# Kernel optimization log

Hardware: AMD Instinct MI355X
Metric: run time of the kernel (lower is better)

Reference implementation:

```python
import jax, jax.numpy as jnp
import numpy as np

N_NODES = 50000
N_EDGES = 800000
IN_FEATS = 128
HIDDEN = 128
NUM_CLASSES = 47


def setup_inputs() -> dict:
    key = jax.random.key(0)
    k1, k2, k3, k4 = jax.random.split(key, 4)
    features = jax.random.normal(k1, (N_NODES, IN_FEATS), dtype=jnp.float32)
    edge_index = jax.random.randint(k2, (2, N_EDGES), 0, N_NODES, dtype=jnp.int32)
    # Glorot-style init for weights, zeros for bias (DGL GraphConv defaults)
    W1 = jax.random.normal(k3, (IN_FEATS, HIDDEN), dtype=jnp.float32) * (1.0 / np.sqrt(IN_FEATS))
    b1 = jnp.zeros((HIDDEN,), dtype=jnp.float32)
    W2 = jax.random.normal(k4, (HIDDEN, NUM_CLASSES), dtype=jnp.float32) * (1.0 / np.sqrt(HIDDEN))
    b2 = jnp.zeros((NUM_CLASSES,), dtype=jnp.float32)
    return {"features": features, "edge_index": edge_index,
            "W1": W1, "b1": b1, "W2": W2, "b2": b2}


def _graph_conv(x, W, b, src, dst, norm_src, norm_dst, n_nodes):
    # DGL GraphConv, norm='both': D_dst^{-1/2} A D_src^{-1/2} (X W) + b
    h = (x * norm_src[:, None]) @ W            # transform before aggregation
    agg = jax.ops.segment_sum(h[src], dst, num_segments=n_nodes)
    return agg * norm_dst[:, None] + b


def reference(features, edge_index, W1, b1, W2, b2):
    src, dst = edge_index[0], edge_index[1]
    n = features.shape[0]
    ones = jnp.ones((src.shape[0],), dtype=features.dtype)
    deg_out = jax.ops.segment_sum(ones, src, num_segments=n)
    deg_in = jax.ops.segment_sum(ones, dst, num_segments=n)
    norm_src = jax.lax.rsqrt(jnp.clip(deg_out, 1.0))   # d_out^{-1/2}, clamp >= 1
    norm_dst = jax.lax.rsqrt(jnp.clip(deg_in, 1.0))    # d_in^{-1/2}, clamp >= 1

    h = _graph_conv(features, W1, b1, src, dst, norm_src, norm_dst, n)
    h = jax.nn.relu(h)
    out = _graph_conv(h, W2, b2, src, dst, norm_src, norm_dst, n)
    return out
```

## Files before the change

kernel.cpp:

```cpp
#include <hip/hip_runtime.h>
#include <hip/hip_fp16.h>

#define N_NODES 50000
#define N_EDGES 800000
#define IN_F 128
#define HID 128
#define NCLS 47
#define H2S 48
#define W2C 64
#define NCH 196
#define NB 128
#define CHUNK 6250
#define PDW 12500
#define G1ROWS 256
#define G2ROWS 128


typedef _Float16 f16x8 __attribute__((ext_vector_type(8)));
typedef float f32x4 __attribute__((ext_vector_type(4)));

struct __align__(8)  h2x2 { __half2 a, b; };
struct __align__(16) h2x4 { __half2 a, b, c, d; };

__global__ __launch_bounds__(256) void prep_kernel(const float* __restrict__ W1,
                                                   const float* __restrict__ W2,
                                                   __half* __restrict__ W1Th,
                                                   __half* __restrict__ W1Tl,
                                                   __half* __restrict__ W2Th,
                                                   __half* __restrict__ W2Tl) {
    const int b = blockIdx.x, t = threadIdx.x;
    if (b < 32) {
        const int i0 = b * 512;
        for (int i2 = i0 + t; i2 < i0 + 512; i2 += 256) {
            int cc = i2 >> 7, k = i2 & 127;
            float w = W1[k * HID + cc];
            __half hv = __float2half_rn(w);
            W1Th[i2] = hv;
            W1Tl[i2] = __float2half_rn(w - __half2float(hv));
        }
    } else {
        const int i0 = (b - 32) * 512;
        for (int i2 = i0 + t; i2 < i0 + 512; i2 += 256) {
            int cc = i2 >> 7, k = i2 & 127;
            float w = (cc < NCLS) ? W2[k * NCLS + cc] : 0.f;
            __half hv = __float2half_rn(w);
            W2Th[i2] = hv;
            W2Tl[i2] = __float2half_rn(w - __half2float(hv));
        }
    }
}

__global__ __launch_bounds__(512) void hist_gemm1_kernel(const int* __restrict__ ei,
        unsigned int* __restrict__ Pdst, unsigned int* __restrict__ Psrc,
        const float* __restrict__ X, const __half* __restrict__ W1Th,
        const __half* __restrict__ W1Tl, __half* __restrict__ H1h) {
    __shared__ unsigned int h[PDW];
    const int t = threadIdx.x;
    if (blockIdx.x < 2 * NB) {
        const bool is_src = blockIdx.x >= NB;
        const int chunk = blockIdx.x & (NB - 1);
        const int* ids = is_src ? ei : ei + N_EDGES;
        uint2* h2 = (uint2*)h;
        for (int j = t; j < PDW / 2; j += 512) h2[j] = make_uint2(0u, 0u);
        __syncthreads();
        const int e0 = chunk * CHUNK;
        const int2* e2p = (const int2*)(ids + e0);
        for (int k = t; k < CHUNK / 2; k += 512) {
            int2 v2 = e2p[k];
            atomicAdd(&h[v2.x >> 2], 1u << ((v2.x & 3) * 8));
            atomicAdd(&h[v2.y >> 2], 1u << ((v2.y & 3) * 8));
        }
        __syncthreads();
        unsigned int* P = (is_src ? Psrc : Pdst) + (size_t)chunk * PDW;
        uint2* P2 = (uint2*)P;
        for (int j = t; j < PDW / 2; j += 512) P2[j] = h2[j];
    } else {
        const int lane = t & 63;
        const int wv = t >> 6;
        const int r16 = lane & 15;
        const int kg = lane >> 4;
        const int row0 = (blockIdx.x - 2 * NB) * G1ROWS + wv * 32;
        f32x4 acc[2][8] = {};
#pragma unroll
        for (int s = 0; s < 4; ++s) {
            const int k0 = 32 * s + 8 * kg;
            f16x8 ah[2], al[2];
#pragma unroll
            for (int rt = 0; rt < 2; ++rt) {
                int row = row0 + rt * 16 + r16;
                int rc = row < N_NODES ? row : N_NODES - 1;
                const float4 x0 = *(const float4*)&X[(size_t)rc * IN_F + k0];
                const float4 x1 = *(const float4*)&X[(size_t)rc * IN_F + k0 + 4];
                const float xv[8] = {x0.x, x0.y, x0.z, x0.w,
                                     x1.x, x1.y, x1.z, x1.w};
#pragma unroll
                for (int j = 0; j < 8; ++j) {
                    _Float16 hv = (_Float16)xv[j];
                    ah[rt][j] = hv;
                    al[rt][j] = (_Float16)(xv[j] - (float)hv);
                }
            }
#pragma unroll
            for (int tt = 0; tt < 8; ++tt) {
                const f16x8 bh = *(const f16x8*)&W1Th[(16 * tt + r16) * IN_F + k0];
                const f16x8 bl = *(const f16x8*)&W1Tl[(16 * tt + r16) * IN_F + k0];
#pragma unroll
                for (int rt = 0; rt < 2; ++rt) {
                    acc[rt][tt] = __builtin_amdgcn_mfma_f32_16x16x32_f16(
                        ah[rt], bh, acc[rt][tt], 0, 0, 0);
                    acc[rt][tt] = __builtin_amdgcn_mfma_f32_16x16x32_f16(
                        al[rt], bh, acc[rt][tt], 0, 0, 0);
                    acc[rt][tt] = __builtin_amdgcn_mfma_f32_16x16x32_f16(
                        ah[rt], bl, acc[rt][tt], 0, 0, 0);
                }
            }
        }
#pragma unroll
        for (int rt = 0; rt < 2; ++rt)
#pragma unroll
            for (int j = 0; j < 4; ++j) {
                const int row = row0 + rt * 16 + 4 * kg + j;
                if (row < N_NODES) {
#pragma unroll
                    for (int tt = 0; tt < 8; ++tt)
                        H1h[(size_t)row * HID + 16 * tt + r16] =
                            __float2half_rn(acc[rt][tt][j]);
                }
            }
    }
}

__global__ __launch_bounds__(256) void reduce_kernel(unsigned int* __restrict__ Pdst,
                                                     const unsigned int* __restrict__ Psrc,
                                                     int* __restrict__ cnt_in,
                                                     float* __restrict__ norm_src,
                                                     float* __restrict__ norm_dst,
                                                     int* __restrict__ chunk_sums) {
    __shared__ int sm[256];
    const int t = threadIdx.x;
    const int j = blockIdx.x * 256 + t;
    int tot = 0;
    if (j < PDW) {
        unsigned int run = 0;
#pragma unroll 8
        for (int b = 0; b < NB; ++b) {
            unsigned int v = Pdst[(size_t)b * PDW + j];
            Pdst[(size_t)b * PDW + j] = run;
            run += v;
        }
        int n0 = run & 0xff, n1 = (run >> 8) & 0xff;
        int n2 = (run >> 16) & 0xff, n3 = (run >> 24) & 0xff;
        *(int4*)&cnt_in[4 * j] = make_int4(n0, n1, n2, n3);
        *(float4*)&norm_dst[4 * j] = make_float4(
            rsqrtf(fmaxf((float)n0, 1.0f)), rsqrtf(fmaxf((float)n1, 1.0f)),
            rsqrtf(fmaxf((float)n2, 1.0f)), rsqrtf(fmaxf((float)n3, 1.0f)));
        tot = n0 + n1 + n2 + n3;
        unsigned int rs = 0;
#pragma unroll 8
        for (int b = 0; b < NB; ++b) rs += Psrc[(size_t)b * PDW + j];
        int s0 = rs & 0xff, s1 = (rs >> 8) & 0xff;
        int s2 = (rs >> 16) & 0xff, s3 = (rs >> 24) & 0xff;
        *(float4*)&norm_src[4 * j] = make_float4(
            rsqrtf(fmaxf((float)s0, 1.0f)), rsqrtf(fmaxf((float)s1, 1.0f)),
            rsqrtf(fmaxf((float)s2, 1.0f)), rsqrtf(fmaxf((float)s3, 1.0f)));
    }
    sm[t] = tot;
    __syncthreads();
    const int g = t & 63;
    for (int off = 32; off > 0; off >>= 1) {
        if (g < off) sm[t] += sm[t + off];
        __syncthreads();
    }
    if (g == 0) chunk_sums[blockIdx.x * 4 + (t >> 6)] = sm[t];
}

__global__ __launch_bounds__(256) void scan3_kernel(const int* __restrict__ cnt_in,
                                                    const int* __restrict__ chunk_sums,
                                                    int* __restrict__ offsets) {
    __shared__ int sm[256];
    const int t = threadIdx.x;
    int v = (t < NCH) ? chunk_sums[t] : 0;
    sm[t] = v;
    __syncthreads();
    for (int off = 1; off < 256; off <<= 1) {
        int u = (t >= off) ? sm[t - off] : 0;
        __syncthreads();
        sm[t] += u;
        __syncthreads();
    }
    const int basev = (blockIdx.x == 0) ? 0 : sm[blockIdx.x - 1];
    __syncthreads();
    const int idx = blockIdx.x * 256 + t;
    int c = (idx < N_NODES) ? cnt_in[idx] : 0;
    sm[t] = c;
    __syncthreads();
    for (int off = 1; off < 256; off <<= 1) {
        int u = (t >= off) ? sm[t - off] : 0;
        __syncthreads();
        sm[t] += u;
        __syncthreads();
    }
    if (idx < N_NODES) offsets[idx] = basev + sm[t] - c;
    if (blockIdx.x == 0 && t == 0) offsets[N_NODES] = N_EDGES;
}

__global__ __launch_bounds__(512) void fill_kernel(const int* __restrict__ src,
        const int* __restrict__ dst, const int* __restrict__ offsets,
        const unsigned int* __restrict__ Pdst, int* __restrict__ csr_src) {
    __shared__ __align__(16) unsigned int cur[PDW];
    const int t = threadIdx.x;
    const int chunk = blockIdx.x;
    uint2* c2 = (uint2*)cur;
    for (int j = t; j < PDW / 2; j += 512) c2[j] = make_uint2(0u, 0u);
    __syncthreads();
    const unsigned int* base = Pdst + (size_t)chunk * PDW;
    const int e0 = chunk * CHUNK;
    const int2* d2p = (const int2*)(dst + e0);
    const int2* s2p = (const int2*)(src + e0);
    for (int k = t; k < CHUNK / 2; k += 512) {
        int2 d2 = d2p[k];
        int2 s2 = s2p[k];
        {
            const int d = d2.x;
            const int sh = (d & 3) * 8;
            const unsigned int bw = base[d >> 2];
            const int off = offsets[d];
            unsigned int old = atomicAdd(&cur[d >> 2], 1u << sh);
            csr_src[off + (int)((bw >> sh) & 0xffu) + (int)((old >> sh) & 0xffu)] = s2.x;
        }
        {
            const int d = d2.y;
            const int sh = (d & 3) * 8;
            const unsigned int bw = base[d >> 2];
            const int off = offsets[d];
            unsigned int old = atomicAdd(&cur[d >> 2], 1u << sh);
            csr_src[off + (int)((bw >> sh) & 0xffu) + (int)((old >> sh) & 0xffu)] = s2.y;
        }
    }
}

__global__ __launch_bounds__(256) void gather1_kernel(const __half* __restrict__ H1h,
        const int* __restrict__ offsets, const int* __restrict__ csr_src,
        const float* __restrict__ b1, const float* __restrict__ norm_src,
        const float* __restrict__ norm_dst, __half* __restrict__ Hrelu16) {
    const int lane = threadIdx.x & 63;
    const int q = lane >> 4;
    const int fl = lane & 15;
    const int row = blockIdx.x * 4 + (threadIdx.x >> 6);
    const int beg = offsets[row], end = offsets[row + 1];
    float a0 = 0.f, a1 = 0.f, a2 = 0.f, a3 = 0.f;
    float a4 = 0.f, a5 = 0.f, a6 = 0.f, a7 = 0.f;
    for (int base = beg; base < end; base += 64) {
        int idx = 0;
        float nsv = 0.f;
        if (base + lane < end) {
            idx = csr_src[base + lane];
            nsv = norm_src[idx];
        }
        const int cnt = min(end - base, 64);
        for (int j = 0; j < cnt; j += 16) {
            int e0 = j + q, e1 = j + 4 + q, e2 = j + 8 + q, e3 = j + 12 + q;
            int s0 = __shfl(idx, e0);  float n0 = __shfl(nsv, e0);
            int s1 = __shfl(idx, e1);  float n1 = __shfl(nsv, e1);
            int s2 = __shfl(idx, e2);  float n2 = __shfl(nsv, e2);
            int s3 = __shfl(idx, e3);  float n3 = __shfl(nsv, e3);
            h2x4 v0 = *(const h2x4*)&H1h[(size_t)s0 * HID + 8 * fl];
            h2x4 v1 = *(const h2x4*)&H1h[(size_t)s1 * HID + 8 * fl];
            h2x4 v2 = *(const h2x4*)&H1h[(size_t)s2 * HID + 8 * fl];
            h2x4 v3 = *(const h2x4*)&H1h[(size_t)s3 * HID + 8 * fl];
            float2 f;
            f = __half22float2(v0.a); a0 = fmaf(f.x, n0, a0); a1 = fmaf(f.y, n0, a1);
            f = __half22float2(v0.b); a2 = fmaf(f.x, n0, a2); a3 = fmaf(f.y, n0, a3);
            f = __half22float2(v0.c); a4 = fmaf(f.x, n0, a4); a5 = fmaf(f.y, n0, a5);
            f = __half22float2(v0.d); a6 = fmaf(f.x, n0, a6); a7 = fmaf(f.y, n0, a7);
            f = __half22float2(v1.a); a0 = fmaf(f.x, n1, a0); a1 = fmaf(f.y, n1, a1);
            f = __half22float2(v1.b); a2 = fmaf(f.x, n1, a2); a3 = fmaf(f.y, n1, a3);
            f = __half22float2(v1.c); a4 = fmaf(f.x, n1, a4); a5 = fmaf(f.y, n1, a5);
            f = __half22float2(v1.d); a6 = fmaf(f.x, n1, a6); a7 = fmaf(f.y, n1, a7);
            f = __half22float2(v2.a); a0 = fmaf(f.x, n2, a0); a1 = fmaf(f.y, n2, a1);
            f = __half22float2(v2.b); a2 = fmaf(f.x, n2, a2); a3 = fmaf(f.y, n2, a3);
            f = __half22float2(v2.c); a4 = fmaf(f.x, n2, a4); a5 = fmaf(f.y, n2, a5);
            f = __half22float2(v2.d); a6 = fmaf(f.x, n2, a6); a7 = fmaf(f.y, n2, a7);
            f = __half22float2(v3.a); a0 = fmaf(f.x, n3, a0); a1 = fmaf(f.y, n3, a1);
            f = __half22float2(v3.b); a2 = fmaf(f.x, n3, a2); a3 = fmaf(f.y, n3, a3);
            f = __half22float2(v3.c); a4 = fmaf(f.x, n3, a4); a5 = fmaf(f.y, n3, a5);
            f = __half22float2(v3.d); a6 = fmaf(f.x, n3, a6); a7 = fmaf(f.y, n3, a7);
        }
    }
    a0 += __shfl_xor(a0, 16); a1 += __shfl_xor(a1, 16);
    a2 += __shfl_xor(a2, 16); a3 += __shfl_xor(a3, 16);
    a4 += __shfl_xor(a4, 16); a5 += __shfl_xor(a5, 16);
    a6 += __shfl_xor(a6, 16); a7 += __shfl_xor(a7, 16);
    a0 += __shfl_xor(a0, 32); a1 += __shfl_xor(a1, 32);
    a2 += __shfl_xor(a2, 32); a3 += __shfl_xor(a3, 32);
    a4 += __shfl_xor(a4, 32); a5 += __shfl_xor(a5, 32);
    a6 += __shfl_xor(a6, 32); a7 += __shfl_xor(a7, 32);
    if (lane < 16) {
        float nd = norm_dst[row], ns = norm_src[row];
        float4 bA = *(const float4*)&b1[8 * fl];
        float4 bB = *(const float4*)&b1[8 * fl + 4];
        float o0 = fmaxf(fmaf(a0, nd, bA.x), 0.f) * ns;
        float o1 = fmaxf(fmaf(a1, nd, bA.y), 0.f) * ns;
        float o2 = fmaxf(fmaf(a2, nd, bA.z), 0.f) * ns;
        float o3 = fmaxf(fmaf(a3, nd, bA.w), 0.f) * ns;
        float o4 = fmaxf(fmaf(a4, nd, bB.x), 0.f) * ns;
        float o5 = fmaxf(fmaf(a5, nd, bB.y), 0.f) * ns;
        float o6 = fmaxf(fmaf(a6, nd, bB.z), 0.f) * ns;
        float o7 = fmaxf(fmaf(a7, nd, bB.w), 0.f) * ns;
        h2x4 p = {__floats2half2_rn(o0, o1), __floats2half2_rn(o2, o3),
                  __floats2half2_rn(o4, o5), __floats2half2_rn(o6, o7)};
        *(h2x4*)&Hrelu16[(size_t)row * HID + 8 * fl] = p;
    }
}

__global__ __launch_bounds__(256) void gemm2_kernel(const __half* __restrict__ Hrelu16,
                                                    const __half* __restrict__ W2Th,
                                                    const __half* __restrict__ W2Tl,
                                                    __half* __restrict__ H2h) {
    const int lane = threadIdx.x & 63;
    const int wv = threadIdx.x >> 6;
    const int r16 = lane & 15;
    const int kg = lane >> 4;
    const int row0 = blockIdx.x * G2ROWS + wv * 32;
    f32x4 acc[2][3] = {};
#pragma unroll
    for (int s = 0; s < 4; ++s) {
        const int k0 = 32 * s + 8 * kg;
        f16x8 a[2];
#pragma unroll
        for (int rt = 0; rt < 2; ++rt) {
            int row = row0 + rt * 16 + r16;
            int rc = row < N_NODES ? row : N_NODES - 1;
            a[rt] = *(const f16x8*)&Hrelu16[(size_t)rc * HID + k0];
        }
#pragma unroll
        for (int tt = 0; tt < 3; ++tt) {
            const f16x8 bh = *(const f16x8*)&W2Th[(16 * tt + r16) * HID + k0];
            const f16x8 bl = *(const f16x8*)&W2Tl[(16 * tt + r16) * HID + k0];
#pragma unroll
            for (int rt = 0; rt < 2; ++rt) {
                acc[rt][tt] = __builtin_amdgcn_mfma_f32_16x16x32_f16(
                    a[rt], bh, acc[rt][tt], 0, 0, 0);
                acc[rt][tt] = __builtin_amdgcn_mfma_f32_16x16x32_f16(
                    a[rt], bl, acc[rt][tt], 0, 0, 0);
            }
        }
    }
#pragma unroll
    for (int rt = 0; rt < 2; ++rt)
#pragma unroll
        for (int j = 0; j < 4; ++j) {
            const int row = row0 + rt * 16 + 4 * kg + j;
            if (row < N_NODES) {
#pragma unroll
                for (int tt = 0; tt < 3; ++tt)
                    H2h[(size_t)row * H2S + 16 * tt + r16] =
                        __float2half_rn(acc[rt][tt][j]);
            }
        }
}

__global__ __launch_bounds__(256) void gather2_kernel(const __half* __restrict__ H2h,
        const int* __restrict__ offsets, const int* __restrict__ csr_src,
        const float* __restrict__ b2, const float* __restrict__ norm_dst,
        float* __restrict__ out) {
    const int lane = threadIdx.x & 63;
    const int row = blockIdx.x * 4 + (threadIdx.x >> 6);
    const int beg = offsets[row], end = offsets[row + 1];
    const int cl = min(lane, H2S - 1);
    float acc = 0.f;
    for (int base = beg; base < end; base += 64) {
        int idx = 0;
        float wv = 0.f;
        if (base + lane < end) {
            idx = csr_src[base + lane];
            wv = 1.f;
        }
        const int cnt = min(end - base, 64);
        for (int j = 0; j < cnt; j += 4) {
            int s0 = __shfl(idx, j);     float w0 = __shfl(wv, j);
            int s1 = __shfl(idx, j + 1); float w1 = __shfl(wv, j + 1);
            int s2 = __shfl(idx, j + 2); float w2 = __shfl(wv, j + 2);
            int s3 = __shfl(idx, j + 3); float w3 = __shfl(wv, j + 3);
            float f0 = __half2float(H2h[(size_t)s0 * H2S + cl]);
            float f1 = __half2float(H2h[(size_t)s1 * H2S + cl]);
            float f2 = __half2float(H2h[(size_t)s2 * H2S + cl]);
            float f3 = __half2float(H2h[(size_t)s3 * H2S + cl]);
            acc = fmaf(f0, w0, acc);
            acc = fmaf(f1, w1, acc);
            acc = fmaf(f2, w2, acc);
            acc = fmaf(f3, w3, acc);
        }
    }
    if (lane < NCLS) out[(size_t)row * NCLS + lane] = acc * norm_dst[row] + b2[lane];
}

extern "C" void kernel_launch(void* const* d_in, const int* in_sizes, int n_in,
                              void* d_out, int out_size, void* d_ws, size_t ws_size,
                              hipStream_t stream) {
    const float* X  = (const float*)d_in[0];
    const int*   ei = (const int*)d_in[1];
    const float* W1 = (const float*)d_in[2];
    const float* b1 = (const float*)d_in[3];
    const float* W2 = (const float*)d_in[4];
    const float* b2 = (const float*)d_in[5];
    float* out = (float*)d_out;

    const int* src = ei;
    const int* dst = ei + N_EDGES;

    char* w = (char*)d_ws;
    auto alloc = [&](size_t bytes) {
        char* p = w;
        w += (bytes + 255) & ~(size_t)255;
        return p;
    };
    float*  norm_src   = (float*)alloc(N_NODES * 4);
    float*  norm_dst   = (float*)alloc(N_NODES * 4);
    int*    cnt_in     = (int*)alloc(N_NODES * 4);
    int*    offsets    = (int*)alloc((N_NODES + 1) * 4);
    int*    csr_src    = (int*)alloc((size_t)N_EDGES * 4);
    int*    chunk_sums = (int*)alloc(NCH * 4);
    __half* W1Th       = (__half*)alloc((size_t)IN_F * HID * 2);
    __half* W1Tl       = (__half*)alloc((size_t)IN_F * HID * 2);
    __half* W2Th       = (__half*)alloc((size_t)W2C * HID * 2);
    __half* W2Tl       = (__half*)alloc((size_t)W2C * HID * 2);
    __half* H1h        = (__half*)alloc((size_t)N_NODES * HID * 2);
    __half* Hrelu16    = (__half*)alloc((size_t)N_NODES * HID * 2);
    __half* H2h        = (__half*)alloc((size_t)N_NODES * H2S * 2);
    unsigned int* Pdst = (unsigned int*)alloc((size_t)NB * PDW * 4);
    unsigned int* Psrc = (unsigned int*)alloc((size_t)NB * PDW * 4);

    const int g1_blocks = (N_NODES + G1ROWS - 1) / G1ROWS;
    const int g2_blocks = (N_NODES + G2ROWS - 1) / G2ROWS;
    prep_kernel<<<48, 256, 0, stream>>>(W1, W2, W1Th, W1Tl, W2Th, W2Tl);
    hist_gemm1_kernel<<<2 * NB + g1_blocks, 512, 0, stream>>>(ei, Pdst, Psrc,
                                                              X, W1Th, W1Tl, H1h);
    reduce_kernel<<<(PDW + 255) / 256, 256, 0, stream>>>(Pdst, Psrc, cnt_in,
                                                         norm_src, norm_dst, chunk_sums);
    scan3_kernel<<<NCH, 256, 0, stream>>>(cnt_in, chunk_sums, offsets);
    fill_kernel<<<NB, 512, 0, stream>>>(src, dst, offsets, Pdst, csr_src);
    gather1_kernel<<<N_NODES / 4, 256, 0, stream>>>(H1h, offsets, csr_src, b1,
                                                    norm_src, norm_dst, Hrelu16);
    gemm2_kernel<<<g2_blocks, 256, 0, stream>>>(Hrelu16, W2Th, W2Tl, H2h);
    gather2_kernel<<<N_NODES / 4, 256, 0, stream>>>(H2h, offsets, csr_src, b2,
                                                    norm_dst, out);
}
```

Measured before the change: 207.2 us.

## Replace chunked shared-memory histograms with global atomic degree count and cursor fill

Drops the per-chunk packed 8-bit shared-memory histograms and their partial-sum reduction. Degrees are now counted with global atomics, and the CSR is filled through a per-node cursor taken from the prefix scan. The fill is fused with GEMM1, which now applies norm_src before storing, so gather1 no longer loads norm_src per edge. This removes large Pdst/Psrc traffic and a reduce pass, in exchange for heavy contention on global atomics and a non-deterministic neighbor order in the CSR.

```diff
diff --git a/kernel.cpp b/kernel.cpp
--- a/kernel.cpp
+++ b/kernel.cpp
@@ -9,12 +9,10 @@
 #define H2S 48
 #define W2C 64
 #define NCH 196
-#define NB 128
-#define CHUNK 6250
-#define PDW 12500
 #define G1ROWS 256
 #define G2ROWS 128
-
+#define DEGB 128
+#define FILLB 256
 
 typedef _Float16 f16x8 __attribute__((ext_vector_type(8)));
 typedef float f32x4 __attribute__((ext_vector_type(4)));
@@ -22,161 +20,72 @@
 struct __align__(8)  h2x2 { __half2 a, b; };
 struct __align__(16) h2x4 { __half2 a, b, c, d; };
 
-__global__ __launch_bounds__(256) void prep_kernel(const float* __restrict__ W1,
-                                                   const float* __restrict__ W2,
-                                                   __half* __restrict__ W1Th,
-                                                   __half* __restrict__ W1Tl,
-                                                   __half* __restrict__ W2Th,
-                                                   __half* __restrict__ W2Tl) {
-    const int b = blockIdx.x, t = threadIdx.x;
-    if (b < 32) {
-        const int i0 = b * 512;
-        for (int i2 = i0 + t; i2 < i0 + 512; i2 += 256) {
-            int cc = i2 >> 7, k = i2 & 127;
-            float w = W1[k * HID + cc];
-            __half hv = __float2half_rn(w);
-            W1Th[i2] = hv;
-            W1Tl[i2] = __float2half_rn(w - __half2float(hv));
+__global__ __launch_bounds__(512) void deg_prep_kernel(const int* __restrict__ ei,
+        int* __restrict__ deg_in, int* __restrict__ deg_out,
+        const float* __restrict__ W1, const float* __restrict__ W2,
+        __half* __restrict__ W1Th, __half* __restrict__ W1Tl,
+        __half* __restrict__ W2Th, __half* __restrict__ W2Tl) {
+    const int t = threadIdx.x;
+    if (blockIdx.x < DEGB) {
+        const int4* s4 = (const int4*)ei;
+        const int4* d4 = (const int4*)(ei + N_EDGES);
+        for (int k = blockIdx.x * 512 + t; k < N_EDGES / 4; k += DEGB * 512) {
+            int4 s = s4[k];
+            int4 d = d4[k];
+            atomicAdd(&deg_out[s.x], 1); atomicAdd(&deg_out[s.y], 1);
+            atomicAdd(&deg_out[s.z], 1); atomicAdd(&deg_out[s.w], 1);
+            atomicAdd(&deg_in[d.x], 1);  atomicAdd(&deg_in[d.y], 1);
+            atomicAdd(&deg_in[d.z], 1);  atomicAdd(&deg_in[d.w], 1);
         }
     } else {
-        const int i0 = (b - 32) * 512;
-        for (int i2 = i0 + t; i2 < i0 + 512; i2 += 256) {
-            int cc = i2 >> 7, k = i2 & 127;
-            float w = (cc < NCLS) ? W2[k * NCLS + cc] : 0.f;
-            __half hv = __float2half_rn(w);
-            W2Th[i2] = hv;
-            W2Tl[i2] = __float2half_rn(w - __half2float(hv));
-        }
-    }
-}
-
-__global__ __launch_bounds__(512) void hist_gemm1_kernel(const int* __restrict__ ei,
-        unsigned int* __restrict__ Pdst, unsigned int* __restrict__ Psrc,
-        const float* __restrict__ X, const __half* __restrict__ W1Th,
-        const __half* __restrict__ W1Tl, __half* __restrict__ H1h) {
-    __shared__ unsigned int h[PDW];
-    const int t = threadIdx.x;
-    if (blockIdx.x < 2 * NB) {
-        const bool is_src = blockIdx.x >= NB;
-        const int chunk = blockIdx.x & (NB - 1);
-        const int* ids = is_src ? ei : ei + N_EDGES;
-        uint2* h2 = (uint2*)h;
-        for (int j = t; j < PDW / 2; j += 512) h2[j] = make_uint2(0u, 0u);
-        __syncthreads();
-        const int e0 = chunk * CHUNK;
-        const int2* e2p = (const int2*)(ids + e0);
-        for (int k = t; k < CHUNK / 2; k += 512) {
-            int2 v2 = e2p[k];
-            atomicAdd(&h[v2.x >> 2], 1u << ((v2.x & 3) * 8));
-            atomicAdd(&h[v2.y >> 2], 1u << ((v2.y & 3) * 8));
-        }
-        __syncthreads();
-        unsigned int* P = (is_src ? Psrc : Pdst) + (size_t)chunk * PDW;
-        uint2* P2 = (uint2*)P;
-        for (int j = t; j < PDW / 2; j += 512) P2[j] = h2[j];
-    } else {
-        const int lane = t & 63;
-        const int wv = t >> 6;
-        const int r16 = lane & 15;
-        const int kg = lane >> 4;
-        const int row0 = (blockIdx.x - 2 * NB) * G1ROWS + wv * 32;
-        f32x4 acc[2][8] = {};
-#pragma unroll
-        for (int s = 0; s < 4; ++s) {
-            const int k0 = 32 * s + 8 * kg;
-            f16x8 ah[2], al[2];
-#pragma unroll
-            for (int rt = 0; rt < 2; ++rt) {
-                int row = row0 + rt * 16 + r16;
-                int rc = row < N_NODES ? row : N_NODES - 1;
-                const float4 x0 = *(const float4*)&X[(size_t)rc * IN_F + k0];
-                const float4 x1 = *(const float4*)&X[(size_t)rc * IN_F + k0 + 4];
-                const float xv[8] = {x0.x, x0.y, x0.z, x0.w,
-                                     x1.x, x1.y, x1.z, x1.w};
-#pragma unroll
-                for (int j = 0; j < 8; ++j) {
-                    _Float16 hv = (_Float16)xv[j];
-                    ah[rt][j] = hv;
-                    al[rt][j] = (_Float16)(xv[j] - (float)hv);
-                }
-            }
-#pragma unroll
-            for (int tt = 0; tt < 8; ++tt) {
-                const f16x8 bh = *(const f16x8*)&W1Th[(16 * tt + r16) * IN_F + k0];
-                const f16x8 bl = *(const f16x8*)&W1Tl[(16 * tt + r16) * IN_F + k0];
-#pragma unroll
-                for (int rt = 0; rt < 2; ++rt) {
-                    acc[rt][tt] = __builtin_amdgcn_mfma_f32_16x16x32_f16(
-                        ah[rt], bh, acc[rt][tt], 0, 0, 0);
-                    acc[rt][tt] = __builtin_amdgcn_mfma_f32_16x16x32_f16(
-                        al[rt], bh, acc[rt][tt], 0, 0, 0);
-                    acc[rt][tt] = __builtin_amdgcn_mfma_f32_16x16x32_f16(
-                        ah[rt], bl, acc[rt][tt], 0, 0, 0);
-                }
-            }
-        }
-#pragma unroll
-        for (int rt = 0; rt < 2; ++rt)
-#pragma unroll
-            for (int j = 0; j < 4; ++j) {
-                const int row = row0 + rt * 16 + 4 * kg + j;
-                if (row < N_NODES) {
-#pragma unroll
-                    for (int tt = 0; tt < 8; ++tt)
-                        H1h[(size_t)row * HID + 16 * tt + r16] =
-                            __float2half_rn(acc[rt][tt][j]);
-                }
-            }
-    }
-}
-
-__global__ __launch_bounds__(256) void reduce_kernel(unsigned int* __restrict__ Pdst,
-                                                     const unsigned int* __restrict__ Psrc,
-                                                     int* __restrict__ cnt_in,
-                                                     float* __restrict__ norm_src,
-                                                     float* __restrict__ norm_dst,
-                                                     int* __restrict__ chunk_sums) {
+        const int pj = blockIdx.x - DEGB;
+        if (pj < 2) {
+            const int i0 = pj * 8192;
+            for (int i2 = i0 + t; i2 < i0 + 8192; i2 += 512) {
+                int cc = i2 >> 7, k = i2 & 127;
+                float w = W1[k * HID + cc];
+                __half hv = __float2half_rn(w);
+                W1Th[i2] = hv;
+                W1Tl[i2] = __float2half_rn(w - __half2float(hv));
+            }
+        } else {
+            for (int i2 = t; i2 < W2C * HID; i2 += 512) {
+                int cc = i2 >> 7, k = i2 & 127;
+                float w = (cc < NCLS) ? W2[k * NCLS + cc] : 0.f;
+                __half hv = __float2half_rn(w);
+                W2Th[i2] = hv;
+                W2Tl[i2] = __float2half_rn(w - __half2float(hv));
+            }
+        }
+    }
+}
+
+__global__ __launch_bounds__(256) void chunksum_kernel(const int* __restrict__ deg_in,
+        const int* __restrict__ deg_out, float* __restrict__ norm_src,
+        float* __restrict__ norm_dst, int* __restrict__ chunk_sums) {
     __shared__ int sm[256];
     const int t = threadIdx.x;
-    const int j = blockIdx.x * 256 + t;
-    int tot = 0;
-    if (j < PDW) {
-        unsigned int run = 0;
-#pragma unroll 8
-        for (int b = 0; b < NB; ++b) {
-            unsigned int v = Pdst[(size_t)b * PDW + j];
-            Pdst[(size_t)b * PDW + j] = run;
-            run += v;
-        }
-        int n0 = run & 0xff, n1 = (run >> 8) & 0xff;
-        int n2 = (run >> 16) & 0xff, n3 = (run >> 24) & 0xff;
-        *(int4*)&cnt_in[4 * j] = make_int4(n0, n1, n2, n3);
-        *(float4*)&norm_dst[4 * j] = make_float4(
-            rsqrtf(fmaxf((float)n0, 1.0f)), rsqrtf(fmaxf((float)n1, 1.0f)),
-            rsqrtf(fmaxf((float)n2, 1.0f)), rsqrtf(fmaxf((float)n3, 1.0f)));
-        tot = n0 + n1 + n2 + n3;
-        unsigned int rs = 0;
-#pragma unroll 8
-        for (int b = 0; b < NB; ++b) rs += Psrc[(size_t)b * PDW + j];
-        int s0 = rs & 0xff, s1 = (rs >> 8) & 0xff;
-        int s2 = (rs >> 16) & 0xff, s3 = (rs >> 24) & 0xff;
-        *(float4*)&norm_src[4 * j] = make_float4(
-            rsqrtf(fmaxf((float)s0, 1.0f)), rsqrtf(fmaxf((float)s1, 1.0f)),
-            rsqrtf(fmaxf((float)s2, 1.0f)), rsqrtf(fmaxf((float)s3, 1.0f)));
-    }
-    sm[t] = tot;
+    const int i = blockIdx.x * 256 + t;
+    int c = 0;
+    if (i < N_NODES) {
+        c = deg_in[i];
+        int o = deg_out[i];
+        norm_dst[i] = rsqrtf(fmaxf((float)c, 1.0f));
+        norm_src[i] = rsqrtf(fmaxf((float)o, 1.0f));
+    }
+    sm[t] = c;
     __syncthreads();
-    const int g = t & 63;
-    for (int off = 32; off > 0; off >>= 1) {
-        if (g < off) sm[t] += sm[t + off];
+    for (int off = 128; off > 0; off >>= 1) {
+        if (t < off) sm[t] += sm[t + off];
         __syncthreads();
     }
-    if (g == 0) chunk_sums[blockIdx.x * 4 + (t >> 6)] = sm[t];
-}
-
-__global__ __launch_bounds__(256) void scan3_kernel(const int* __restrict__ cnt_in,
+    if (t == 0) chunk_sums[blockIdx.x] = sm[0];
+}
+
+__global__ __launch_bounds__(256) void scan3_kernel(const int* __restrict__ deg_in,
                                                     const int* __restrict__ chunk_sums,
-                                                    int* __restrict__ offsets) {
+                                                    int* __restrict__ offsets,
+                                                    int* __restrict__ cursor) {
     __shared__ int sm[256];
     const int t = threadIdx.x;
     int v = (t < NCH) ? chunk_sums[t] : 0;
@@ -191,7 +100,7 @@
     const int basev = (blockIdx.x == 0) ? 0 : sm[blockIdx.x - 1];
     __syncthreads();
     const int idx = blockIdx.x * 256 + t;
-    int c = (idx < N_NODES) ? cnt_in[idx] : 0;
+    int c = (idx < N_NODES) ? deg_in[idx] : 0;
     sm[t] = c;
     __syncthreads();
     for (int off = 1; off < 256; off <<= 1) {
@@ -200,42 +109,90 @@
         sm[t] += u;
         __syncthreads();
     }
-    if (idx < N_NODES) offsets[idx] = basev + sm[t] - c;
+    if (idx < N_NODES) {
+        int o = basev + sm[t] - c;
+        offsets[idx] = o;
+        cursor[idx] = o;
+    }
     if (blockIdx.x == 0 && t == 0) offsets[N_NODES] = N_EDGES;
 }
 
-__global__ __launch_bounds__(512) void fill_kernel(const int* __restrict__ src,
-        const int* __restrict__ dst, const int* __restrict__ offsets,
-        const unsigned int* __restrict__ Pdst, int* __restrict__ csr_src) {
-    __shared__ __align__(16) unsigned int cur[PDW];
+__global__ __launch_bounds__(512) void fill_gemm1_kernel(const int* __restrict__ ei,
+        int* __restrict__ cursor, int* __restrict__ csr_src,
+        const float* __restrict__ X, const float* __restrict__ norm_src,
+        const __half* __restrict__ W1Th, const __half* __restrict__ W1Tl,
+        __half* __restrict__ H1h) {
     const int t = threadIdx.x;
-    const int chunk = blockIdx.x;
-    uint2* c2 = (uint2*)cur;
-    for (int j = t; j < PDW / 2; j += 512) c2[j] = make_uint2(0u, 0u);
-    __syncthreads();
-    const unsigned int* base = Pdst + (size_t)chunk * PDW;
-    const int e0 = chunk * CHUNK;
-    const int2* d2p = (const int2*)(dst + e0);
-    const int2* s2p = (const int2*)(src + e0);
-    for (int k = t; k < CHUNK / 2; k += 512) {
-        int2 d2 = d2p[k];
-        int2 s2 = s2p[k];
-        {
-            const int d = d2.x;
-            const int sh = (d & 3) * 8;
-            const unsigned int bw = base[d >> 2];
-            const int off = offsets[d];
-            unsigned int old = atomicAdd(&cur[d >> 2], 1u << sh);
-            csr_src[off + (int)((bw >> sh) & 0xffu) + (int)((old >> sh) & 0xffu)] = s2.x;
-        }
-        {
-            const int d = d2.y;
-            const int sh = (d & 3) * 8;
-            const unsigned int bw = base[d >> 2];
-            const int off = offsets[d];
-            unsigned int old = atomicAdd(&cur[d >> 2], 1u << sh);
-            csr_src[off + (int)((bw >> sh) & 0xffu) + (int)((old >> sh) & 0xffu)] = s2.y;
-        }
+    if (blockIdx.x >= 196) {
+        const int b = blockIdx.x - 196;
+        const int4* s4 = (const int4*)ei;
+        const int4* d4 = (const int4*)(ei + N_EDGES);
+        for (int k = b * 512 + t; k < N_EDGES / 4; k += FILLB * 512) {
+            int4 s = s4[k];
+            int4 d = d4[k];
+            int o0 = atomicAdd(&cursor[d.x], 1);
+            int o1 = atomicAdd(&cursor[d.y], 1);
+            int o2 = atomicAdd(&cursor[d.z], 1);
+            int o3 = atomicAdd(&cursor[d.w], 1);
+            csr_src[o0] = s.x;
+            csr_src[o1] = s.y;
+            csr_src[o2] = s.z;
+            csr_src[o3] = s.w;
+        }
+    } else {
+        const int lane = t & 63;
+        const int wv = t >> 6;
+        const int r16 = lane & 15;
+        const int kg = lane >> 4;
+        const int row0 = blockIdx.x * G1ROWS + wv * 32;
+        f32x4 acc[2][8] = {};
+#pragma unroll
+        for (int s = 0; s < 4; ++s) {
+            const int k0 = 32 * s + 8 * kg;
+            f16x8 ah[2], al[2];
+#pragma unroll
+            for (int rt = 0; rt < 2; ++rt) {
+                int row = row0 + rt * 16 + r16;
+                int rc = row < N_NODES ? row : N_NODES - 1;
+                const float4 x0 = *(const float4*)&X[(size_t)rc * IN_F + k0];
+                const float4 x1 = *(const float4*)&X[(size_t)rc * IN_F + k0 + 4];
+                const float xv[8] = {x0.x, x0.y, x0.z, x0.w,
+                                     x1.x, x1.y, x1.z, x1.w};
+#pragma unroll
+                for (int j = 0; j < 8; ++j) {
+                    _Float16 hv = (_Float16)xv[j];
+                    ah[rt][j] = hv;
+                    al[rt][j] = (_Float16)(xv[j] - (float)hv);
+                }
+            }
+#pragma unroll
+            for (int tt = 0; tt < 8; ++tt) {
+                const f16x8 bh = *(const f16x8*)&W1Th[(16 * tt + r16) * IN_F + k0];
+                const f16x8 bl = *(const f16x8*)&W1Tl[(16 * tt + r16) * IN_F + k0];
+#pragma unroll
+                for (int rt = 0; rt < 2; ++rt) {
+                    acc[rt][tt] = __builtin_amdgcn_mfma_f32_16x16x32_f16(
+                        ah[rt], bh, acc[rt][tt], 0, 0, 0);
+                    acc[rt][tt] = __builtin_amdgcn_mfma_f32_16x16x32_f16(
+                        al[rt], bh, acc[rt][tt], 0, 0, 0);
+                    acc[rt][tt] = __builtin_amdgcn_mfma_f32_16x16x32_f16(
+                        ah[rt], bl, acc[rt][tt], 0, 0, 0);
+                }
+            }
+        }
+#pragma unroll
+        for (int rt = 0; rt < 2; ++rt)
+#pragma unroll
+            for (int j = 0; j < 4; ++j) {
+                const int row = row0 + rt * 16 + 4 * kg + j;
+                if (row < N_NODES) {
+                    const float nsr = norm_src[row];
+#pragma unroll
+                    for (int tt = 0; tt < 8; ++tt)
+                        H1h[(size_t)row * HID + 16 * tt + r16] =
+                            __float2half_rn(acc[rt][tt][j] * nsr);
+                }
+            }
     }
 }
 
@@ -252,18 +209,18 @@
     float a4 = 0.f, a5 = 0.f, a6 = 0.f, a7 = 0.f;
     for (int base = beg; base < end; base += 64) {
         int idx = 0;
-        float nsv = 0.f;
+        float wv = 0.f;
         if (base + lane < end) {
             idx = csr_src[base + lane];
-            nsv = norm_src[idx];
+            wv = 1.f;
         }
         const int cnt = min(end - base, 64);
         for (int j = 0; j < cnt; j += 16) {
             int e0 = j + q, e1 = j + 4 + q, e2 = j + 8 + q, e3 = j + 12 + q;
-            int s0 = __shfl(idx, e0);  float n0 = __shfl(nsv, e0);
-            int s1 = __shfl(idx, e1);  float n1 = __shfl(nsv, e1);
-            int s2 = __shfl(idx, e2);  float n2 = __shfl(nsv, e2);
-            int s3 = __shfl(idx, e3);  float n3 = __shfl(nsv, e3);
+            int s0 = __shfl(idx, e0);  float n0 = __shfl(wv, e0);
+            int s1 = __shfl(idx, e1);  float n1 = __shfl(wv, e1);
+            int s2 = __shfl(idx, e2);  float n2 = __shfl(wv, e2);
+            int s3 = __shfl(idx, e3);  float n3 = __shfl(wv, e3);
             h2x4 v0 = *(const h2x4*)&H1h[(size_t)s0 * HID + 8 * fl];
             h2x4 v1 = *(const h2x4*)&H1h[(size_t)s1 * HID + 8 * fl];
             h2x4 v2 = *(const h2x4*)&H1h[(size_t)s2 * HID + 8 * fl];
@@ -406,18 +363,18 @@
     const float* b2 = (const float*)d_in[5];
     float* out = (float*)d_out;
 
-    const int* src = ei;
-    const int* dst = ei + N_EDGES;
-
     char* w = (char*)d_ws;
     auto alloc = [&](size_t bytes) {
         char* p = w;
         w += (bytes + 255) & ~(size_t)255;
         return p;
     };
+    int*    deg        = (int*)alloc((size_t)2 * N_NODES * 4);
+    int*    deg_in     = deg;
+    int*    deg_out    = deg + N_NODES;
+    int*    cursor     = (int*)alloc(N_NODES * 4);
     float*  norm_src   = (float*)alloc(N_NODES * 4);
     float*  norm_dst   = (float*)alloc(N_NODES * 4);
-    int*    cnt_in     = (int*)alloc(N_NODES * 4);
     int*    offsets    = (int*)alloc((N_NODES + 1) * 4);
     int*    csr_src    = (int*)alloc((size_t)N_EDGES * 4);
     int*    chunk_sums = (int*)alloc(NCH * 4);
@@ -428,18 +385,19 @@
     __half* H1h        = (__half*)alloc((size_t)N_NODES * HID * 2);
     __half* Hrelu16    = (__half*)alloc((size_t)N_NODES * HID * 2);
     __half* H2h        = (__half*)alloc((size_t)N_NODES * H2S * 2);
-    unsigned int* Pdst = (unsigned int*)alloc((size_t)NB * PDW * 4);
-    unsigned int* Psrc = (unsigned int*)alloc((size_t)NB * PDW * 4);
 
     const int g1_blocks = (N_NODES + G1ROWS - 1) / G1ROWS;
     const int g2_blocks = (N_NODES + G2ROWS - 1) / G2ROWS;
-    prep_kernel<<<48, 256, 0, stream>>>(W1, W2, W1Th, W1Tl, W2Th, W2Tl);
-    hist_gemm1_kernel<<<2 * NB + g1_blocks, 512, 0, stream>>>(ei, Pdst, Psrc,
-                                                              X, W1Th, W1Tl, H1h);
-    reduce_kernel<<<(PDW + 255) / 256, 256, 0, stream>>>(Pdst, Psrc, cnt_in,
-                                                         norm_src, norm_dst, chunk_sums);
-    scan3_kernel<<<NCH, 256, 0, stream>>>(cnt_in, chunk_sums, offsets);
-    fill_kernel<<<NB, 512, 0, stream>>>(src, dst, offsets, Pdst, csr_src);
+
+    hipMemsetAsync(deg, 0, (size_t)2 * N_NODES * 4, stream);
+    deg_prep_kernel<<<DEGB + 3, 512, 0, stream>>>(ei, deg_in, deg_out, W1, W2,
+                                                  W1Th, W1Tl, W2Th, W2Tl);
+    chunksum_kernel<<<NCH, 256, 0, stream>>>(deg_in, deg_out, norm_src,
+                                             norm_dst, chunk_sums);
+    scan3_kernel<<<NCH, 256, 0, stream>>>(deg_in, chunk_sums, offsets, cursor);
+    fill_gemm1_kernel<<<196 + FILLB, 512, 0, stream>>>(ei, cursor, csr_src,
+                                                       X, norm_src,
+                                                       W1Th, W1Tl, H1h);
     gather1_kernel<<<N_NODES / 4, 256, 0, stream>>>(H1h, offsets, csr_src, b1,
                                                     norm_src, norm_dst, Hrelu16);
     gemm2_kernel<<<g2_blocks, 256, 0, stream>>>(Hrelu16, W2Th, W2Tl, H2h);
```

Measured after the change: 268.1 us. +29.4%, slower.
